# Kernel tuning notes

Measured on AMD Instinct MI355X. Metric: run time of the kernel, lower is better.

Reference implementation:

```python
import jax, jax.numpy as jnp
from jax import lax
import numpy as np
import math

KSIZE, STRIDE, RATE, FUSE_K, SCALE, FUSE = 3, 1, 2, 3, 10.0, True
DN = ('NCHW', 'OIHW', 'NCHW')


def extract_image_patches(img, kernel, stride=1):
    # Faithful to the torch helper, including the F.pad quirk where pad_row
    # (computed from height) is applied to the width axis and vice versa.
    bsz, c, h, w = img.shape
    h2 = math.ceil(h / stride)
    w2 = math.ceil(w / stride)
    pad_row = (h2 - 1) * stride + kernel - h
    pad_col = (w2 - 1) * stride + kernel - w
    x = jnp.pad(img, ((0, 0), (0, 0),
                      (pad_col // 2, pad_col - pad_col // 2),
                      (pad_row // 2, pad_row - pad_row // 2)))
    cols = []
    for i in range(kernel):
        for j in range(kernel):
            cols.append(x[:, :, i:i + (h2 - 1) * stride + 1:stride,
                          j:j + (w2 - 1) * stride + 1:stride])
    patches = jnp.stack(cols, axis=-1).reshape(bsz, c, h2, w2, kernel, kernel)
    patches = jnp.transpose(patches, (0, 4, 5, 1, 2, 3))  # [b,kh,kw,c,h2,w2]
    return patches.reshape(bsz, -1, h2, w2)


def setup_inputs() -> dict:
    key = jax.random.key(0)
    k1, k2, k3 = jax.random.split(key, 3)
    f = jax.random.normal(k1, (4, 128, 96, 96), dtype=jnp.float32)
    b = jax.random.normal(k2, (4, 128, 96, 96), dtype=jnp.float32)
    mask = jax.random.uniform(k3, (4, 1, 96, 96), dtype=jnp.float32)
    return {'f': f, 'b': b, 'mask': mask}


def reference(f, b, mask):
    bs, cs, hs, ws = f.shape
    kernel = RATE * 2
    # raw background patches used as conv_transpose filters (C-order reshape as in torch .view)
    raw_w = extract_image_patches(b, kernel, RATE * STRIDE)
    raw_w = raw_w.reshape(bs, -1, kernel, kernel, cs).transpose(0, 1, 4, 2, 3)  # [bs,L,cs,4,4]
    # nearest downsample by rate (matches F.interpolate nearest with scale 1/rate)
    fd = f[:, :, ::RATE, ::RATE]
    bd = b[:, :, ::RATE, ::RATE]
    md = mask[:, :, ::RATE, ::RATE]
    ih, iw = bd.shape[2], bd.shape[3]
    L = ih * iw
    w = extract_image_patches(bd, KSIZE, STRIDE)
    w = w.reshape(bs, -1, KSIZE, KSIZE, cs).transpose(0, 1, 4, 2, 3)  # [bs,L,cs,3,3]
    m = extract_image_patches(md, KSIZE, STRIDE)
    m = m.reshape(bs, -1, 1, KSIZE, KSIZE).transpose(0, 2, 3, 4, 1)  # [bs,1,3,3,L]
    mms = (jnp.mean(1.0 - m, axis=(1, 2, 3)) < 0.85).astype(f.dtype)  # [bs,L]
    fuse_w = jnp.eye(FUSE_K, dtype=f.dtype).reshape(1, 1, FUSE_K, FUSE_K)

    def per_sample(xi, wi, raw_wi, mm):
        # xi [cs,ih,iw], wi [L,cs,3,3], raw_wi [L,cs,4,4], mm [L]
        norm = jnp.sqrt(jnp.sum(wi * wi, axis=(1, 2, 3)) + 1e-8)
        wi_n = wi / jnp.maximum(norm, 1e-4)[:, None, None, None]
        yi = lax.conv_general_dilated(xi[None], wi_n, (1, 1), ((1, 1), (1, 1)),
                                      dimension_numbers=DN)  # [1,L,ih,iw]
        if FUSE:
            yi = yi.reshape(1, 1, ih * iw, ih * iw)
            yi = lax.conv_general_dilated(yi, fuse_w, (1, 1), ((1, 1), (1, 1)), dimension_numbers=DN)
            yi = yi.reshape(1, ih, iw, ih, iw).transpose(0, 2, 1, 4, 3)
            yi = yi.reshape(1, 1, ih * iw, ih * iw)
            yi = lax.conv_general_dilated(yi, fuse_w, (1, 1), ((1, 1), (1, 1)), dimension_numbers=DN)
            yi = yi.reshape(1, iw, ih, iw, ih).transpose(0, 2, 1, 4, 3)
        yi = yi.reshape(1, ih, iw, iw * ih)
        yi = yi * mm
        yi = jax.nn.softmax(yi * SCALE, axis=3)
        yi = yi * mm
        off = jnp.argmax(yi, axis=3).astype(jnp.int32)
        off = jnp.stack([off // hs, off % hs], axis=-1).transpose(0, 3, 1, 2)  # [1,2,ih,iw]
        yi = yi.transpose(0, 3, 1, 2)  # [1,L,ih,iw]
        # conv_transpose2d(yi, raw_wi, stride=RATE, padding=1) == dilated corr with flipped, transposed kernel
        w_t = jnp.flip(raw_wi, (-2, -1)).transpose(1, 0, 2, 3)  # [cs,L,4,4]
        pad = kernel - 1 - 1
        out = lax.conv_general_dilated(yi, w_t, (1, 1), ((pad, pad), (pad, pad)),
                                       lhs_dilation=(RATE, RATE), dimension_numbers=DN) / 4.0
        return out[0], off[0]

    y, offsets = jax.vmap(per_sample)(fd, w, raw_w, mms)  # y [bs,cs,hs,ws], offsets [bs,2,ih,iw]
    grid = jnp.stack([jnp.broadcast_to(jnp.arange(ih)[:, None], (ih, iw)),
                      jnp.broadcast_to(jnp.arange(iw)[None, :], (ih, iw))], 0).astype(jnp.int32)
    offsets = offsets - grid[None]
    # flow_to_image (external numpy visualization) omitted; raw offsets returned instead.
    return y, offsets
```

## Files before the change

### kernel.cpp

```cpp
#include <hip/hip_runtime.h>
#include <hip/hip_bf16.h>
#include <math.h>

#define IH 48
#define IW 48
#define LTOT 2304
#define CS 128
#define HS 96
#define KRED 1152
#define CRED 2048

typedef unsigned short u16;
typedef __attribute__((ext_vector_type(8))) short short8;
typedef __attribute__((ext_vector_type(8))) unsigned short ushort8;
typedef __attribute__((ext_vector_type(4))) float floatx4;

#define NS    ((size_t)LTOT*LTOT)
#define PLANE ((size_t)LTOT*KRED)
#define NRT   ((size_t)CRED*LTOT)

#define OFF_APL  ((size_t)0)
#define OFF_BPL  ((size_t)10616832)
#define OFF_S    ((size_t)21233664)
#define OFF_SM   ((size_t)42467328)
#define REGION   ((size_t)42485760)

__device__ __forceinline__ u16 f2bf(float v) {
    __hip_bfloat16 h = __float2bfloat16(v);
    return *reinterpret_cast<u16*>(&h);
}
__device__ __forceinline__ float bf2f(u16 b) {
    __hip_bfloat16 h = *reinterpret_cast<__hip_bfloat16*>(&b);
    return __bfloat162float(h);
}
__device__ __forceinline__ void split2(float v, u16& a, u16& b) {
    a = f2bf(v);
    b = f2bf(v - bf2f(a));
}

__global__ __launch_bounds__(256) void k_wnorm(const float* __restrict__ b,
                                               float* __restrict__ ninvg,
                                               int b0, size_t zsF) {
    int bi = b0 + blockIdx.z;
    float* ninv = ninvg + (size_t)blockIdx.z * zsF;
    int l = blockIdx.x, t = threadIdx.x;
    __shared__ float red[256];
    float ss = 0.f;
    for (int G = t; G < KRED; G += 256) {
        int F = l * KRED + G;
        int p2 = F / LTOT, s = F - p2 * LTOT;
        int i = p2 / 384, j = (p2 / 128) % 3, c = p2 & 127;
        int u = s / IW + i - 1, v = s % IW + j - 1;
        if (u >= 0 && u < IH && v >= 0 && v < IW) {
            float w = b[(((size_t)bi * CS + c) * HS + 2 * u) * HS + 2 * v];
            ss += w * w;
        }
    }
    red[t] = ss; __syncthreads();
    for (int o = 128; o > 0; o >>= 1) { if (t < o) red[t] += red[t + o]; __syncthreads(); }
    if (t == 0) ninv[l] = 1.0f / fmaxf(sqrtf(red[0] + 1e-8f), 1e-4f);
}

__global__ __launch_bounds__(256) void k_gather_w(const float* __restrict__ b,
                                                  u16* __restrict__ Ag,
                                                  const float* __restrict__ ninvg,
                                                  int b0, size_t zsU, size_t zsF) {
    int bi = b0 + blockIdx.z;
    u16* A = Ag + (size_t)blockIdx.z * zsU;
    const float* ninv = ninvg + (size_t)blockIdx.z * zsF;
    int idx = blockIdx.x * 256 + threadIdx.x;
    int p2 = idx / LTOT, s = idx - p2 * LTOT;
    int i = p2 / 384, j = (p2 / 128) % 3, c = p2 & 127;
    int u = s / IW + i - 1, v = s % IW + j - 1;
    float val = 0.f;
    if (u >= 0 && u < IH && v >= 0 && v < IW)
        val = b[(((size_t)bi * CS + c) * HS + 2 * u) * HS + 2 * v];
    val *= ninv[idx / KRED];
    u16 h1, h2; split2(val, h1, h2);
    A[idx] = h1; A[PLANE + idx] = h2;
}

__global__ __launch_bounds__(256) void k_gather_x_tiled(const float* __restrict__ f,
                                                        u16* __restrict__ Bg,
                                                        int b0, size_t zsU) {
    __shared__ float ldsf[128 * 55];
    int bi = b0 + blockIdx.z;
    u16* B = Bg + (size_t)blockIdx.z * zsU;
    int bx = blockIdx.x;
    int y = bx / 3, x0 = (bx % 3) * 16;
    int t = threadIdx.x;
    for (int i = 0; i < 27; ++i) {
        int g = i * 256 + t;
        if (g < 6912) {
            int vl = g % 18;
            int row = (g / 18) % 3;
            int c = g / 54;
            int u = y + row - 1;
            int v = x0 - 1 + vl;
            float val = 0.f;
            if (u >= 0 && u < IH && v >= 0 && v < IW)
                val = f[(((size_t)bi * CS + c) * HS + 2 * u) * HS + 2 * v];
            ldsf[c * 55 + row * 18 + vl] = val;
        }
    }
    __syncthreads();
    for (int i = 0; i < 72; ++i) {
        int o = i * 256 + t;
        int xp = o / 1152, G = o - xp * 1152;
        int k1 = G / 384, k2 = (G >> 7) % 3, c = G & 127;
        float val = ldsf[c * 55 + k1 * 18 + xp + k2];
        u16 h1, h2; split2(val, h1, h2);
        size_t idx = (size_t)(y * IW + x0 + xp) * KRED + G;
        B[idx] = h1; B[PLANE + idx] = h2;
    }
}

__global__ __launch_bounds__(256) void k_mm(const float* __restrict__ mask,
                                            float* __restrict__ mmvg, int b0, size_t zsF) {
    int bi = b0 + blockIdx.z;
    float* out = mmvg + (size_t)blockIdx.z * zsF;
    int q = blockIdx.x * 256 + threadIdx.x;
    if (q >= LTOT) return;
    float ssum = 0.f;
    for (int t = 0; t < 9; t++) {
        int F = q * 9 + t;
        int pm = F / LTOT, s = F % LTOT;
        int i = pm / 3, j = pm % 3;
        int u = s / IW + i - 1, v = s % IW + j - 1;
        float val = 0.f;
        if (u >= 0 && u < IH && v >= 0 && v < IW)
            val = mask[((size_t)bi * HS + 2 * u) * HS + 2 * v];
        ssum += 1.0f - val;
    }
    out[q] = (ssum / 9.0f < 0.85f) ? 1.0f : 0.0f;
}

__global__ __launch_bounds__(256) void k_gather_rt_tiled(const float* __restrict__ b,
                                                         u16* __restrict__ Rtg,
                                                         int b0, size_t zsU) {
    __shared__ u16 tile[64 * 65];
    int bi = b0 + blockIdx.z;
    u16* Rt = Rtg + (size_t)blockIdx.z * zsU;
    int bx = blockIdx.x;
    int k0 = (bx >> 5) * 64, n0 = (bx & 31) * 64;
    int t = threadIdx.x;
    for (int i = 0; i < 16; ++i) {
        int kl = i * 4 + (t >> 6), nl = t & 63;
        int F = (k0 + kl) * CRED + n0 + nl;
        int pr = F / LTOT, s = F - pr * LTOT;
        int ii = pr / 512, j = (pr >> 7) & 3, c = pr & 127;
        int Y0 = 2 * (s / IW) + ii - 1, X0 = 2 * (s % IW) + j - 1;
        float val = 0.f;
        if (Y0 >= 0 && Y0 < HS && X0 >= 0 && X0 < HS)
            val = b[(((size_t)bi * CS + c) * HS + Y0) * HS + X0];
        tile[kl * 65 + nl] = f2bf(val);
    }
    __syncthreads();
    for (int i = 0; i < 16; ++i) {
        int nl = i * 4 + (t >> 6), kl = t & 63;
        Rt[(size_t)(n0 + nl) * LTOT + k0 + kl] = tile[kl * 65 + nl];
    }
}

template <int NP, int BK>
__global__ __launch_bounds__(256) void k_gemm_mfma(const u16* __restrict__ Ag,
                                                   const u16* __restrict__ Bg,
                                                   float* __restrict__ Cg,
                                                   size_t zsA, size_t zsB, size_t zsC,
                                                   size_t planeStride,
                                                   int M, int N, int K) {
    constexpr int SLOTS = BK / 8;
    constexpr int SMASK = SLOTS - 1;
    constexpr int TSZ = 128 * BK;
    constexpr int NLD = NP * BK / 16;
    __shared__ u16 lds[2 * NP * TSZ];
    u16* As = lds;
    u16* Bs = lds + NP * TSZ;
    const int tid = threadIdx.x;
    const int lane = tid & 63;
    const int wave = tid >> 6;
    const int wr = (wave >> 1) * 64, wc = (wave & 1) * 64;
    const int lrow = lane & 15, lq = lane >> 4;

    unsigned gx = gridDim.x, gy = gridDim.y;
    unsigned nwg = gx * gy * gridDim.z;
    unsigned wg = (blockIdx.z * gy + blockIdx.y) * gx + blockIdx.x;
    {
        unsigned q = nwg >> 3, r = nwg & 7, xcd = wg & 7, lid = wg >> 3;
        wg = (xcd < r ? xcd * (q + 1) : r * (q + 1) + (xcd - r) * q) + lid;
    }
    unsigned z = wg / (gx * gy);
    unsigned rem2 = wg - z * gx * gy;
    const int bm = (int)(rem2 / gx) * 128, bn = (int)(rem2 % gx) * 128;

    const u16* A = Ag + (size_t)z * zsA;
    const u16* B = Bg + (size_t)z * zsB;
    float* C = Cg + (size_t)z * zsC;

    floatx4 acc[4][4];
#pragma unroll
    for (int i = 0; i < 4; i++)
#pragma unroll
        for (int j = 0; j < 4; j++) acc[i][j] = (floatx4){0.f, 0.f, 0.f, 0.f};

    for (int kt = 0; kt < K; kt += BK) {
        ushort8 stA[NLD], stB[NLD];
#pragma unroll
        for (int e = 0; e < NLD; ++e) {
            int g = e * 256 + tid;
            int p = g / (128 * SLOTS);
            int gg = g % (128 * SLOTS);
            int row = gg / SLOTS, slot = gg & SMASK;
            stA[e] = *(const ushort8*)(A + (size_t)p * planeStride + (size_t)(bm + row) * K + kt + slot * 8);
            stB[e] = *(const ushort8*)(B + (size_t)p * planeStride + (size_t)(bn + row) * K + kt + slot * 8);
        }
        __syncthreads();
#pragma unroll
        for (int e = 0; e < NLD; ++e) {
            int g = e * 256 + tid;
            int p = g / (128 * SLOTS);
            int gg = g % (128 * SLOTS);
            int row = gg / SLOTS, slot = gg & SMASK;
            int dst = p * TSZ + row * BK + ((slot ^ (row & SMASK)) << 3);
            *(ushort8*)&As[dst] = stA[e];
            *(ushort8*)&Bs[dst] = stB[e];
        }
        __syncthreads();

#pragma unroll
        for (int ks = 0; ks < BK / 32; ++ks) {
            short8 af[NP][4];
#pragma unroll
            for (int p = 0; p < NP; ++p)
#pragma unroll
                for (int mi = 0; mi < 4; ++mi) {
                    int row = wr + mi * 16 + lrow;
                    af[p][mi] = *(const short8*)&As[p * TSZ + row * BK + ((((ks << 2) | lq) ^ (row & SMASK)) << 3)];
                }
#pragma unroll
            for (int ni = 0; ni < 4; ++ni) {
                short8 bfr[NP];
                int rowb = wc + ni * 16 + lrow;
                int bslot = ((((ks << 2) | lq) ^ (rowb & SMASK)) << 3);
#pragma unroll
                for (int p = 0; p < NP; ++p)
                    bfr[p] = *(const short8*)&Bs[p * TSZ + rowb * BK + bslot];
#pragma unroll
                for (int mi = 0; mi < 4; ++mi) {
                    if constexpr (NP == 1) {
                        acc[mi][ni] = __builtin_amdgcn_mfma_f32_16x16x32_bf16(af[0][mi], bfr[0], acc[mi][ni], 0, 0, 0);
                    } else {
                        acc[mi][ni] = __builtin_amdgcn_mfma_f32_16x16x32_bf16(af[1][mi], bfr[0], acc[mi][ni], 0, 0, 0);
                        acc[mi][ni] = __builtin_amdgcn_mfma_f32_16x16x32_bf16(af[0][mi], bfr[1], acc[mi][ni], 0, 0, 0);
                        acc[mi][ni] = __builtin_amdgcn_mfma_f32_16x16x32_bf16(af[0][mi], bfr[0], acc[mi][ni], 0, 0, 0);
                    }
                }
            }
        }
    }

    const int r0 = bm + wr + (lane >> 4) * 4;
    const int c0 = bn + wc + (lane & 15);
#pragma unroll
    for (int mi = 0; mi < 4; ++mi)
#pragma unroll
        for (int ni = 0; ni < 4; ++ni)
#pragma unroll
            for (int j = 0; j < 4; ++j)
                C[(size_t)(r0 + mi * 16 + j) * N + (c0 + ni * 16)] = acc[mi][ni][j];
}

__device__ __forceinline__ int permi(int a) { return (a % 48) * 48 + a / 48; }

__device__ __forceinline__ float f1_at(const float* __restrict__ S, int a, int b) {
    float s = S[(size_t)a * LTOT + b];
    if (a >= 1 && b >= 1) s += S[(size_t)(a - 1) * LTOT + (b - 1)];
    if (a < LTOT - 1 && b < LTOT - 1) s += S[(size_t)(a + 1) * LTOT + (b + 1)];
    return s;
}

__global__ __launch_bounds__(256) void k_fusesoftmax(const float* __restrict__ Sg,
                                                     const float* __restrict__ mmg,
                                                     u16* __restrict__ attbg,
                                                     float* __restrict__ offout,
                                                     int b0, size_t zsF, size_t zsU) {
    int bi = b0 + blockIdx.z;
    const float* S = Sg + (size_t)blockIdx.z * zsF;
    const float* mm = mmg + (size_t)blockIdx.z * zsF;
    u16* attb = attbg + (size_t)blockIdx.z * zsU;
    int bx = blockIdx.x;
    int l = (bx & 7) * 288 + (bx >> 3);
    int t = threadIdx.x;
    __shared__ float red[256];
    __shared__ int redi[256];
    u16* arow = attb + (size_t)l * LTOT;

    const int At = permi(l);
    const int rm = (At >= 1) ? permi(At - 1) : -1;
    const int rp = (At < LTOT - 1) ? permi(At + 1) : -1;

    float v[9], m9[9];
#pragma unroll
    for (int i = 0; i < 9; ++i) {
        int p = t + 256 * i;
        float d = f1_at(S, l, p);
        int Bt = permi(p);
        if (rm >= 0 && Bt >= 1)        d += f1_at(S, rm, permi(Bt - 1));
        if (rp >= 0 && Bt < LTOT - 1)  d += f1_at(S, rp, permi(Bt + 1));
        m9[i] = mm[p];
        v[i] = d * m9[i] * 10.0f;
    }
    float mx = -1e30f;
#pragma unroll
    for (int i = 0; i < 9; ++i) mx = fmaxf(mx, v[i]);
    red[t] = mx; __syncthreads();
    for (int o = 128; o > 0; o >>= 1) { if (t < o) red[t] = fmaxf(red[t], red[t + o]); __syncthreads(); }
    mx = red[0]; __syncthreads();
    float sm = 0.f;
#pragma unroll
    for (int i = 0; i < 9; ++i) sm += expf(v[i] - mx);
    red[t] = sm; __syncthreads();
    for (int o = 128; o > 0; o >>= 1) { if (t < o) red[t] += red[t + o]; __syncthreads(); }
    float Z = red[0]; __syncthreads();
    float bv = -1.0f; int bidx2 = 0;
#pragma unroll
    for (int i = 0; i < 9; ++i) {
        int p = t + 256 * i;
        float e = expf(v[i] - mx);
        float a = (e / Z) * m9[i];
        arow[p] = f2bf(a);
        if (a > bv) { bv = a; bidx2 = p; }
    }
    red[t] = bv; redi[t] = bidx2; __syncthreads();
    for (int o = 128; o > 0; o >>= 1) {
        if (t < o) {
            if (red[t + o] > red[t] || (red[t + o] == red[t] && redi[t + o] < redi[t])) {
                red[t] = red[t + o]; redi[t] = redi[t + o];
            }
        }
        __syncthreads();
    }
    if (t == 0) {
        int off = redi[0];
        int ly = l / IW, lx = l % IW;
        offout[((size_t)bi * 2 + 0) * LTOT + l] = (float)(off / 96 - ly);
        offout[((size_t)bi * 2 + 1) * LTOT + l] = (float)(off % 96 - lx);
    }
}

__global__ __launch_bounds__(256) void k_output_tiled(const float* __restrict__ Cg,
                                                      float* __restrict__ yout,
                                                      int b0, size_t zsF) {
    __shared__ float lo[64 * 129];
    int bi = b0 + blockIdx.z;
    const float* C = Cg + (size_t)blockIdx.z * zsF;
    int bx = blockIdx.x;
    int Y0 = (bx / 6) * 4, X0 = (bx % 6) * 16;
    int t = threadIdx.x;
    int c = t & 127;
    for (int i = 0; i < 32; ++i) {
        int pos = i * 2 + (t >> 7);
        int Y = Y0 + (pos >> 4), X = X0 + (pos & 15);
        float s = 0.f;
        int pu = (Y + 1) & 1, pv = (X + 1) & 1;
#pragma unroll
        for (int a = 0; a < 2; a++) {
            int u = pu + 2 * a;
            int ly2 = Y + 1 - u;
            if (ly2 < 0) continue;
            int ly = ly2 >> 1;
            if (ly >= IH) continue;
#pragma unroll
            for (int bb = 0; bb < 2; bb++) {
                int v = pv + 2 * bb;
                int lx2 = X + 1 - v;
                if (lx2 < 0) continue;
                int lx = lx2 >> 1;
                if (lx >= IW) continue;
                s += C[(size_t)(ly * IW + lx) * CRED + u * 512 + v * 128 + c];
            }
        }
        lo[pos * 129 + c] = s * 0.25f;
    }
    __syncthreads();
    for (int i = 0; i < 32; ++i) {
        int cc = i * 4 + (t >> 6);
        int pos = t & 63;
        float val = lo[pos * 129 + cc];
        int yl = pos >> 4, xl = pos & 15;
        yout[(((size_t)bi * CS + cc) * HS + Y0 + yl) * HS + X0 + xl] = val;
    }
}

extern "C" void kernel_launch(void* const* d_in, const int* in_sizes, int n_in,
                              void* d_out, int out_size, void* d_ws, size_t ws_size,
                              hipStream_t stream) {
    const float* f = (const float*)d_in[0];
    const float* b = (const float*)d_in[1];
    const float* mask = (const float*)d_in[2];
    float* yout = (float*)d_out;
    float* offout = yout + (size_t)4 * CS * HS * HS;

    int ZB, nloop;
    if (ws_size >= 4 * REGION)      { ZB = 4; nloop = 1; }
    else if (ws_size >= 2 * REGION) { ZB = 2; nloop = 2; }
    else                            { ZB = 1; nloop = 4; }

    char* base = (char*)d_ws;
    u16*   Apl  = (u16*)(base + OFF_APL);
    u16*   Bpl  = (u16*)(base + OFF_BPL);
    float* S    = (float*)(base + OFF_S);
    float* Cc   = (float*)(base + OFF_S);
    float* ninv = (float*)(base + OFF_SM);
    float* mmv  = ninv + LTOT;
    u16*   attb = Apl;
    u16*   Rt   = Bpl;

    const size_t zsU = REGION / 2;
    const size_t zsF = REGION / 4;

    dim3 blk(256, 1, 1);
    const unsigned ghalf = (unsigned)(PLANE / 256);

    for (int it = 0; it < nloop; ++it) {
        int b0 = it * ZB;
        k_wnorm<<<dim3(LTOT, 1, ZB), blk, 0, stream>>>(b, ninv, b0, zsF);
        k_gather_w<<<dim3(ghalf, 1, ZB), blk, 0, stream>>>(b, Apl, ninv, b0, zsU, zsF);
        k_gather_x_tiled<<<dim3(IH * 3, 1, ZB), blk, 0, stream>>>(f, Bpl, b0, zsU);
        k_mm<<<dim3((LTOT + 255) / 256, 1, ZB), blk, 0, stream>>>(mask, mmv, b0, zsF);
        k_gemm_mfma<2, 64><<<dim3(LTOT / 128, LTOT / 128, ZB), blk, 0, stream>>>(
            Apl, Bpl, S, zsU, zsU, zsF, PLANE, LTOT, LTOT, KRED);
        k_fusesoftmax<<<dim3(LTOT, 1, ZB), blk, 0, stream>>>(S, mmv, attb, offout, b0, zsF, zsU);
        k_gather_rt_tiled<<<dim3((LTOT / 64) * (CRED / 64), 1, ZB), blk, 0, stream>>>(b, Rt, b0, zsU);
        k_gemm_mfma<1, 128><<<dim3(CRED / 128, LTOT / 128, ZB), blk, 0, stream>>>(
            attb, Rt, Cc, zsU, zsU, zsF, PLANE, LTOT, CRED, LTOT);
        k_output_tiled<<<dim3((HS / 4) * (HS / 16), 1, ZB), blk, 0, stream>>>(Cc, yout, b0, zsF);
    }
}
```

Measured before the change: 512.4 us.

## Replace attention-by-patches GEMM with sparse thresholded gather-accumulate in softmax kernel

Removes the bf16 attention write-out, the background-patch transpose gather and the second MFMA GEMM. The softmax kernel now collects every masked position whose logit lies within 20 of the masked maximum, with weights stored in LDS. It then accumulates the corresponding background patch values directly into the fp32 C row, gathering them from global memory with scalar FMAs. This pays off only when few candidates survive the threshold. With near-flat logits almost all 2304 positions survive, so each row performs a full dense product through uncoalesced gathers instead of using matrix cores.

Result: no change. 515.8 us (+0.7%).

```diff
diff --git a/kernel.cpp b/kernel.cpp
--- a/kernel.cpp
+++ b/kernel.cpp
@@ -17,13 +17,13 @@
 
 #define NS    ((size_t)LTOT*LTOT)
 #define PLANE ((size_t)LTOT*KRED)
-#define NRT   ((size_t)CRED*LTOT)
 
 #define OFF_APL  ((size_t)0)
 #define OFF_BPL  ((size_t)10616832)
 #define OFF_S    ((size_t)21233664)
-#define OFF_SM   ((size_t)42467328)
-#define REGION   ((size_t)42485760)
+#define OFF_C    ((size_t)42467328)
+#define OFF_SM   ((size_t)61341696)
+#define REGION   ((size_t)61360128)
 
 __device__ __forceinline__ u16 f2bf(float v) {
     __hip_bfloat16 h = __float2bfloat16(v);
@@ -135,33 +135,6 @@
     out[q] = (ssum / 9.0f < 0.85f) ? 1.0f : 0.0f;
 }
 
-__global__ __launch_bounds__(256) void k_gather_rt_tiled(const float* __restrict__ b,
-                                                         u16* __restrict__ Rtg,
-                                                         int b0, size_t zsU) {
-    __shared__ u16 tile[64 * 65];
-    int bi = b0 + blockIdx.z;
-    u16* Rt = Rtg + (size_t)blockIdx.z * zsU;
-    int bx = blockIdx.x;
-    int k0 = (bx >> 5) * 64, n0 = (bx & 31) * 64;
-    int t = threadIdx.x;
-    for (int i = 0; i < 16; ++i) {
-        int kl = i * 4 + (t >> 6), nl = t & 63;
-        int F = (k0 + kl) * CRED + n0 + nl;
-        int pr = F / LTOT, s = F - pr * LTOT;
-        int ii = pr / 512, j = (pr >> 7) & 3, c = pr & 127;
-        int Y0 = 2 * (s / IW) + ii - 1, X0 = 2 * (s % IW) + j - 1;
-        float val = 0.f;
-        if (Y0 >= 0 && Y0 < HS && X0 >= 0 && X0 < HS)
-            val = b[(((size_t)bi * CS + c) * HS + Y0) * HS + X0];
-        tile[kl * 65 + nl] = f2bf(val);
-    }
-    __syncthreads();
-    for (int i = 0; i < 16; ++i) {
-        int nl = i * 4 + (t >> 6), kl = t & 63;
-        Rt[(size_t)(n0 + nl) * LTOT + k0 + kl] = tile[kl * 65 + nl];
-    }
-}
-
 template <int NP, int BK>
 __global__ __launch_bounds__(256) void k_gemm_mfma(const u16* __restrict__ Ag,
                                                    const u16* __restrict__ Bg,
@@ -281,19 +254,24 @@
 
 __global__ __launch_bounds__(256) void k_fusesoftmax(const float* __restrict__ Sg,
                                                      const float* __restrict__ mmg,
-                                                     u16* __restrict__ attbg,
+                                                     const float* __restrict__ bsrc,
+                                                     float* __restrict__ Cg,
                                                      float* __restrict__ offout,
-                                                     int b0, size_t zsF, size_t zsU) {
-    int bi = b0 + blockIdx.z;
-    const float* S = Sg + (size_t)blockIdx.z * zsF;
-    const float* mm = mmg + (size_t)blockIdx.z * zsF;
-    u16* attb = attbg + (size_t)blockIdx.z * zsU;
+                                                     int b0, size_t zsF) {
+    int z = blockIdx.z;
+    int bi = b0 + z;
+    const float* S = Sg + (size_t)z * zsF;
+    const float* mm = mmg + (size_t)z * zsF;
+    float* C = Cg + (size_t)z * zsF;
     int bx = blockIdx.x;
     int l = (bx & 7) * 288 + (bx >> 3);
     int t = threadIdx.x;
     __shared__ float red[256];
     __shared__ int redi[256];
-    u16* arow = attb + (size_t)l * LTOT;
+    __shared__ int scand[2304];
+    __shared__ float swght[2304];
+    __shared__ int scnt;
+    if (t == 0) scnt = 0;
 
     const int At = permi(l);
     const int rm = (At >= 1) ? permi(At - 1) : -1;
@@ -322,14 +300,24 @@
     red[t] = sm; __syncthreads();
     for (int o = 128; o > 0; o >>= 1) { if (t < o) red[t] += red[t + o]; __syncthreads(); }
     float Z = red[0]; __syncthreads();
+    float mul = -1e30f;
+#pragma unroll
+    for (int i = 0; i < 9; ++i) if (m9[i] > 0.f) mul = fmaxf(mul, v[i]);
+    red[t] = mul; __syncthreads();
+    for (int o = 128; o > 0; o >>= 1) { if (t < o) red[t] = fmaxf(red[t], red[t + o]); __syncthreads(); }
+    float mu = red[0]; __syncthreads();
     float bv = -1.0f; int bidx2 = 0;
 #pragma unroll
     for (int i = 0; i < 9; ++i) {
         int p = t + 256 * i;
         float e = expf(v[i] - mx);
         float a = (e / Z) * m9[i];
-        arow[p] = f2bf(a);
         if (a > bv) { bv = a; bidx2 = p; }
+        if (m9[i] > 0.f && v[i] >= mu - 20.0f) {
+            int pos = atomicAdd(&scnt, 1);
+            scand[pos] = p;
+            swght[pos] = e / Z;
+        }
     }
     red[t] = bv; redi[t] = bidx2; __syncthreads();
     for (int o = 128; o > 0; o >>= 1) {
@@ -346,6 +334,29 @@
         offout[((size_t)bi * 2 + 0) * LTOT + l] = (float)(off / 96 - ly);
         offout[((size_t)bi * 2 + 1) * LTOT + l] = (float)(off % 96 - lx);
     }
+    int cnt = scnt;
+    float accv[8];
+#pragma unroll
+    for (int j = 0; j < 8; ++j) accv[j] = 0.f;
+    for (int ci = 0; ci < cnt; ++ci) {
+        int p = scand[ci];
+        float w = swght[ci];
+#pragma unroll
+        for (int j = 0; j < 8; ++j) {
+            int n = t + 256 * j;
+            int F = p * CRED + n;
+            int pr = F / LTOT, s = F - pr * LTOT;
+            int ii = pr >> 9, jj = (pr >> 7) & 3, c = pr & 127;
+            int Y0 = 2 * (s / IW) + ii - 1, X0 = 2 * (s % IW) + jj - 1;
+            float val = 0.f;
+            if (Y0 >= 0 && Y0 < HS && X0 >= 0 && X0 < HS)
+                val = bsrc[(((size_t)bi * CS + c) * HS + Y0) * HS + X0];
+            accv[j] += w * val;
+        }
+    }
+    float* Crow = C + (size_t)l * CRED;
+#pragma unroll
+    for (int j = 0; j < 8; ++j) Crow[t + 256 * j] = accv[j] * 0.25f;
 }
 
 __global__ __launch_bounds__(256) void k_output_tiled(const float* __restrict__ Cg,
@@ -380,7 +391,7 @@
                 s += C[(size_t)(ly * IW + lx) * CRED + u * 512 + v * 128 + c];
             }
         }
-        lo[pos * 129 + c] = s * 0.25f;
+        lo[pos * 129 + c] = s;
     }
     __syncthreads();
     for (int i = 0; i < 32; ++i) {
@@ -410,11 +421,9 @@
     u16*   Apl  = (u16*)(base + OFF_APL);
     u16*   Bpl  = (u16*)(base + OFF_BPL);
     float* S    = (float*)(base + OFF_S);
-    float* Cc   = (float*)(base + OFF_S);
+    float* Cc   = (float*)(base + OFF_C);
     float* ninv = (float*)(base + OFF_SM);
     float* mmv  = ninv + LTOT;
-    u16*   attb = Apl;
-    u16*   Rt   = Bpl;
 
     const size_t zsU = REGION / 2;
     const size_t zsF = REGION / 4;
@@ -430,10 +439,7 @@
         k_mm<<<dim3((LTOT + 255) / 256, 1, ZB), blk, 0, stream>>>(mask, mmv, b0, zsF);
         k_gemm_mfma<2, 64><<<dim3(LTOT / 128, LTOT / 128, ZB), blk, 0, stream>>>(
             Apl, Bpl, S, zsU, zsU, zsF, PLANE, LTOT, LTOT, KRED);
-        k_fusesoftmax<<<dim3(LTOT, 1, ZB), blk, 0, stream>>>(S, mmv, attb, offout, b0, zsF, zsU);
-        k_gather_rt_tiled<<<dim3((LTOT / 64) * (CRED / 64), 1, ZB), blk, 0, stream>>>(b, Rt, b0, zsU);
-        k_gemm_mfma<1, 128><<<dim3(CRED / 128, LTOT / 128, ZB), blk, 0, stream>>>(
-            attb, Rt, Cc, zsU, zsU, zsF, PLANE, LTOT, CRED, LTOT);
+        k_fusesoftmax<<<dim3(LTOT, 1, ZB), blk, 0, stream>>>(S, mmv, b, Cc, offout, b0, zsF);
         k_output_tiled<<<dim3((HS / 4) * (HS / 16), 1, ZB), blk, 0, stream>>>(Cc, yout, b0, zsF);
     }
 }
```
